# Optimization experiments

Hardware: AMD Instinct MI355X
Metric: run time of the kernel (lower is better)

Reference implementation:

```python
import jax, jax.numpy as jnp
import numpy as np

N = 8192
IN_C = 128
OUT_C = 64
ALPHA = 0.5  # LeakyReLU negative slope
NEG_INF = -9e15


def _xavier(key, shape, gain=1.414):
    fan_in, fan_out = shape[0], shape[-1]
    bound = gain * np.sqrt(6.0 / (fan_in + fan_out))
    return jax.random.uniform(key, shape, jnp.float32, -bound, bound)


def setup_inputs() -> dict:
    key = jax.random.key(0)
    k1, k2, k3, k4 = jax.random.split(key, 4)
    h = jax.random.normal(k1, (N, IN_C), jnp.float32)
    adj = jax.random.randint(k2, (N, N), 0, 2, jnp.int32)
    W = _xavier(k3, (IN_C, OUT_C))
    a = _xavier(k4, (2 * OUT_C, 1))
    return {"h": h, "adj": adj, "W": W, "a": a}


def reference(h, adj, W, a):
    # Wh: [N, out]
    Wh = h @ W
    a1 = a[:OUT_C, 0]   # [out]
    a2 = a[OUT_C:, 0]   # [out]
    # additive attention score e[i, j] = leakyrelu((Wh a1)_i + (Wh a2)_j)
    e = jax.nn.leaky_relu(
        (Wh @ a1)[:, None] + (Wh @ a2)[None, :], negative_slope=ALPHA
    )  # [N, N]
    scores = jnp.where(adj > 0, e, NEG_INF)
    attention = jax.nn.softmax(scores, axis=1)  # masked row softmax
    h_prime = attention @ Wh                    # [N, out]
    return jax.nn.leaky_relu(h_prime, negative_slope=ALPHA)  # concat=True path
```

## Files before the change

kernel.cpp:

```cpp
#include <hip/hip_runtime.h>
#include <hip/hip_bf16.h>

#define NN 8192
#define INC 128
#define OUTC 64

typedef __attribute__((ext_vector_type(8))) short bf16x8;
typedef __attribute__((ext_vector_type(4))) float f32x4;
typedef __attribute__((ext_vector_type(4))) int i32x4;

static __device__ __forceinline__ unsigned short f2bf(float x) {
    unsigned int u = __builtin_bit_cast(unsigned int, x);
    u += 0x7fffu + ((u >> 16) & 1u);
    return (unsigned short)(u >> 16);
}
static __device__ __forceinline__ float bf2f(unsigned short b) {
    unsigned int u = ((unsigned int)b) << 16;
    return __builtin_bit_cast(float, u);
}

__global__ __launch_bounds__(256) void k1_wh(const float* __restrict__ h,
                                             const float* __restrict__ W,
                                             const float* __restrict__ a,
                                             unsigned short* __restrict__ whbt,
                                             float* __restrict__ f,
                                             float* __restrict__ g)
{
    const int gid = blockIdx.x * 256 + threadIdx.x;
    const int row = gid >> 6;
    const int ch  = gid & 63;
    const f32x4* h4 = (const f32x4*)(h + (size_t)row * INC);
    float acc = 0.f;
#pragma unroll 8
    for (int k4 = 0; k4 < INC / 4; ++k4) {
        f32x4 hv = h4[k4];
        acc += hv[0] * W[(k4 * 4 + 0) * OUTC + ch];
        acc += hv[1] * W[(k4 * 4 + 1) * OUTC + ch];
        acc += hv[2] * W[(k4 * 4 + 2) * OUTC + ch];
        acc += hv[3] * W[(k4 * 4 + 3) * OUTC + ch];
    }
    whbt[(size_t)ch * NN + row] = f2bf(acc);

    float v1 = acc * a[ch];
    float v2 = acc * a[64 + ch];
#pragma unroll
    for (int m = 1; m < 64; m <<= 1) {
        v1 += __shfl_xor(v1, m, 64);
        v2 += __shfl_xor(v2, m, 64);
    }
    if ((threadIdx.x & 63) == 0) {
        f[row] = v1;
        g[row] = v2;
    }
}

__global__ __launch_bounds__(256) void k2_gmax(const float* __restrict__ g,
                                               float* __restrict__ gmax)
{
    __shared__ float red[256];
    float m = -1e30f;
    for (int i = threadIdx.x; i < NN; i += 256) m = fmaxf(m, g[i]);
    red[threadIdx.x] = m;
    __syncthreads();
    for (int s = 128; s > 0; s >>= 1) {
        if ((int)threadIdx.x < s) red[threadIdx.x] = fmaxf(red[threadIdx.x], red[threadIdx.x + s]);
        __syncthreads();
    }
    if (threadIdx.x == 0) *gmax = red[0];
}

__global__ __launch_bounds__(256) void k3_attn(const int* __restrict__ adj,
                                               const unsigned short* __restrict__ whbt,
                                               const float* __restrict__ f,
                                               const float* __restrict__ g,
                                               const float* __restrict__ gmaxp,
                                               float* __restrict__ accP,
                                               float* __restrict__ lP,
                                               int colsPerChunk)
{
    const int lane = threadIdx.x & 63;
    const int wave = threadIdx.x >> 6;
    const int lr16 = lane & 15;
    const int kg   = lane >> 4;
    const int rowBase = blockIdx.x * 64 + wave * 16;
    const int r = rowBase + lr16;
    const int chunk = blockIdx.y;
    const int jStart = chunk * colsPerChunk;

    const float L2E = 1.4426950408889634f;
    const float fr = f[r];
    const float gmax = *gmaxp;
    float mm = fr + gmax;
    mm = fmaxf(mm, 0.5f * mm);
    const float mL = mm * L2E;

    f32x4 acc0 = {0.f, 0.f, 0.f, 0.f};
    f32x4 acc1 = {0.f, 0.f, 0.f, 0.f};
    f32x4 acc2 = {0.f, 0.f, 0.f, 0.f};
    f32x4 acc3 = {0.f, 0.f, 0.f, 0.f};
    float ls = 0.f;

    const int* adjRow = adj + (size_t)r * NN;
    const unsigned short* wb0 = whbt + (size_t)(0 * 16 + lr16) * NN;
    const unsigned short* wb1 = whbt + (size_t)(1 * 16 + lr16) * NN;
    const unsigned short* wb2 = whbt + (size_t)(2 * 16 + lr16) * NN;
    const unsigned short* wb3 = whbt + (size_t)(3 * 16 + lr16) * NN;

    for (int j0 = jStart; j0 < jStart + colsPerChunk; j0 += 32) {
        const int jl = j0 + kg * 8;
        i32x4 ad0 = *(const i32x4*)(adjRow + jl);
        i32x4 ad1 = *(const i32x4*)(adjRow + jl + 4);
        f32x4 g0  = *(const f32x4*)(g + jl);
        f32x4 g1  = *(const f32x4*)(g + jl + 4);
        bf16x8 b0 = *(const bf16x8*)(wb0 + jl);
        bf16x8 b1 = *(const bf16x8*)(wb1 + jl);
        bf16x8 b2 = *(const bf16x8*)(wb2 + jl);
        bf16x8 b3 = *(const bf16x8*)(wb3 + jl);

        bf16x8 af;
#pragma unroll
        for (int t = 0; t < 8; ++t) {
            float gj = (t < 4) ? g0[t] : g1[t - 4];
            int   ad = (t < 4) ? ad0[t] : ad1[t - 4];
            float s  = fr + gj;
            float lr = fmaxf(s, 0.5f * s);
            float w  = __builtin_amdgcn_exp2f(lr * L2E - mL);
            w = (ad > 0) ? w : 0.f;
            unsigned short b = f2bf(w);
            af[t] = (short)b;
            ls += bf2f(b);
        }
        acc0 = __builtin_amdgcn_mfma_f32_16x16x32_bf16(af, b0, acc0, 0, 0, 0);
        acc1 = __builtin_amdgcn_mfma_f32_16x16x32_bf16(af, b1, acc1, 0, 0, 0);
        acc2 = __builtin_amdgcn_mfma_f32_16x16x32_bf16(af, b2, acc2, 0, 0, 0);
        acc3 = __builtin_amdgcn_mfma_f32_16x16x32_bf16(af, b3, acc3, 0, 0, 0);
    }

    ls += __shfl_xor(ls, 16, 64);
    ls += __shfl_xor(ls, 32, 64);
    if (lane < 16) lP[(size_t)chunk * NN + rowBase + lane] = ls;

    float* ap = accP + (size_t)chunk * NN * OUTC;
#pragma unroll
    for (int q = 0; q < 4; ++q) {
        const int rm = rowBase + kg * 4 + q;
        ap[(size_t)rm * OUTC +  0 + lr16] = acc0[q];
        ap[(size_t)rm * OUTC + 16 + lr16] = acc1[q];
        ap[(size_t)rm * OUTC + 32 + lr16] = acc2[q];
        ap[(size_t)rm * OUTC + 48 + lr16] = acc3[q];
    }
}

__global__ __launch_bounds__(256) void k4_final(const float* __restrict__ accP,
                                                const float* __restrict__ lP,
                                                float* __restrict__ out, int js)
{
    const int gid = blockIdx.x * 256 + threadIdx.x;
    const int row = gid >> 6;
    const int ch  = gid & 63;
    float av = 0.f, lv = 0.f;
    for (int c = 0; c < js; ++c) {
        av += accP[((size_t)c * NN + row) * OUTC + ch];
        lv += lP[(size_t)c * NN + row];
    }
    if (lv == 0.f) lv = 1.f;
    const float hv = av / lv;
    out[(size_t)row * OUTC + ch] = fmaxf(hv, 0.5f * hv);
}

extern "C" void kernel_launch(void* const* d_in, const int* in_sizes, int n_in,
                              void* d_out, int out_size, void* d_ws, size_t ws_size,
                              hipStream_t stream)
{
    const float* h   = (const float*)d_in[0];
    const int*   adj = (const int*)d_in[1];
    const float* W   = (const float*)d_in[2];
    const float* a   = (const float*)d_in[3];
    float* out = (float*)d_out;

    char* ws = (char*)d_ws;
    unsigned short* whbt = (unsigned short*)ws;
    size_t off = (size_t)OUTC * NN * sizeof(unsigned short);
    float* f = (float*)(ws + off); off += (size_t)NN * 4;
    float* g = (float*)(ws + off); off += (size_t)NN * 4;
    float* gmax = (float*)(ws + off); off += 256;

    const size_t perChunk = (size_t)NN * OUTC * 4 + (size_t)NN * 4;
    int js = 8;
    while (js > 1 && off + (size_t)js * perChunk > ws_size) js >>= 1;
    float* accP = (float*)(ws + off); off += (size_t)js * NN * OUTC * 4;
    float* lP   = (float*)(ws + off);

    k1_wh<<<dim3(NN * OUTC / 256), 256, 0, stream>>>(h, W, a, whbt, f, g);
    k2_gmax<<<1, 256, 0, stream>>>(g, gmax);
    const int colsPerChunk = NN / js;
    k3_attn<<<dim3(NN / 64, js), 256, 0, stream>>>(adj, whbt, f, g, gmax, accP, lP, colsPerChunk);
    k4_final<<<dim3(NN * OUTC / 256), 256, 0, stream>>>(accP, lP, out, js);
}
```

Baseline: 462.6 us.

## Pack adjacency into bitmask before attention kernel and coalesce Wh transpose stores

Adds a pre-pass that reads the int32 adjacency matrix once and packs it into a bitmask. The attention kernel then reads one 32-bit word per 32 columns instead of 32 ints, which cuts its adjacency traffic. k1 now transposes through shared memory so its Wh stores are vectorised, the column split doubles to 16 chunks, and the main loop is unrolled by 2. The full int32 adjacency is still read once, plus a 8 MB mask is written and read back, and k4 now has to reduce more partial chunks.

```diff
diff --git a/kernel.cpp b/kernel.cpp
--- a/kernel.cpp
+++ b/kernel.cpp
@@ -17,6 +17,28 @@
 static __device__ __forceinline__ float bf2f(unsigned short b) {
     unsigned int u = ((unsigned int)b) << 16;
     return __builtin_bit_cast(float, u);
+}
+
+__global__ __launch_bounds__(256) void ka_pack(const int* __restrict__ adj,
+                                               unsigned long long* __restrict__ msk)
+{
+    const int lane = threadIdx.x & 63;
+    const int wid  = (blockIdx.x * 256 + threadIdx.x) >> 6;
+    const int l16  = lane & 15;
+    const int g16  = lane >> 4;
+#pragma unroll 4
+    for (int i = 0; i < 32; ++i) {
+        const size_t base = ((size_t)wid * 32 + i) * 256;
+        i32x4 v = *(const i32x4*)(adj + base + 4 * lane);
+        unsigned int nib = (v[0] > 0 ? 1u : 0u) | (v[1] > 0 ? 2u : 0u)
+                         | (v[2] > 0 ? 4u : 0u) | (v[3] > 0 ? 8u : 0u);
+        unsigned long long m = (unsigned long long)nib << (4 * l16);
+        m |= __shfl_xor(m, 1, 64);
+        m |= __shfl_xor(m, 2, 64);
+        m |= __shfl_xor(m, 4, 64);
+        m |= __shfl_xor(m, 8, 64);
+        if (l16 == 0) msk[base / 64 + g16] = m;
+    }
 }
 
 __global__ __launch_bounds__(256) void k1_wh(const float* __restrict__ h,
@@ -26,9 +48,9 @@
                                              float* __restrict__ f,
                                              float* __restrict__ g)
 {
-    const int gid = blockIdx.x * 256 + threadIdx.x;
-    const int row = gid >> 6;
-    const int ch  = gid & 63;
+    const int wave = threadIdx.x >> 6;
+    const int ch   = threadIdx.x & 63;
+    const int row  = blockIdx.x * 4 + wave;
     const f32x4* h4 = (const f32x4*)(h + (size_t)row * INC);
     float acc = 0.f;
 #pragma unroll 8
@@ -39,7 +61,8 @@
         acc += hv[2] * W[(k4 * 4 + 2) * OUTC + ch];
         acc += hv[3] * W[(k4 * 4 + 3) * OUTC + ch];
     }
-    whbt[(size_t)ch * NN + row] = f2bf(acc);
+    __shared__ unsigned short tr[64][4];
+    tr[ch][wave] = f2bf(acc);
 
     float v1 = acc * a[ch];
     float v2 = acc * a[64 + ch];
@@ -48,9 +71,11 @@
         v1 += __shfl_xor(v1, m, 64);
         v2 += __shfl_xor(v2, m, 64);
     }
-    if ((threadIdx.x & 63) == 0) {
-        f[row] = v1;
-        g[row] = v2;
+    if (ch == 0) { f[row] = v1; g[row] = v2; }
+    __syncthreads();
+    if (wave == 0) {
+        ushort4 o = *(const ushort4*)&tr[ch][0];
+        *(ushort4*)(whbt + (size_t)ch * NN + blockIdx.x * 4) = o;
     }
 }
 
@@ -69,7 +94,7 @@
     if (threadIdx.x == 0) *gmax = red[0];
 }
 
-__global__ __launch_bounds__(256) void k3_attn(const int* __restrict__ adj,
+__global__ __launch_bounds__(256) void k3_attn(const unsigned int* __restrict__ msk,
                                                const unsigned short* __restrict__ whbt,
                                                const float* __restrict__ f,
                                                const float* __restrict__ g,
@@ -100,16 +125,17 @@
     f32x4 acc3 = {0.f, 0.f, 0.f, 0.f};
     float ls = 0.f;
 
-    const int* adjRow = adj + (size_t)r * NN;
+    const unsigned int* mrow = msk + (size_t)r * (NN / 32);
     const unsigned short* wb0 = whbt + (size_t)(0 * 16 + lr16) * NN;
     const unsigned short* wb1 = whbt + (size_t)(1 * 16 + lr16) * NN;
     const unsigned short* wb2 = whbt + (size_t)(2 * 16 + lr16) * NN;
     const unsigned short* wb3 = whbt + (size_t)(3 * 16 + lr16) * NN;
 
+#pragma unroll 2
     for (int j0 = jStart; j0 < jStart + colsPerChunk; j0 += 32) {
         const int jl = j0 + kg * 8;
-        i32x4 ad0 = *(const i32x4*)(adjRow + jl);
-        i32x4 ad1 = *(const i32x4*)(adjRow + jl + 4);
+        unsigned int mw = mrow[j0 >> 5];
+        unsigned int myb = (mw >> (kg * 8)) & 0xffu;
         f32x4 g0  = *(const f32x4*)(g + jl);
         f32x4 g1  = *(const f32x4*)(g + jl + 4);
         bf16x8 b0 = *(const bf16x8*)(wb0 + jl);
@@ -121,11 +147,10 @@
 #pragma unroll
         for (int t = 0; t < 8; ++t) {
             float gj = (t < 4) ? g0[t] : g1[t - 4];
-            int   ad = (t < 4) ? ad0[t] : ad1[t - 4];
             float s  = fr + gj;
             float lr = fmaxf(s, 0.5f * s);
             float w  = __builtin_amdgcn_exp2f(lr * L2E - mL);
-            w = (ad > 0) ? w : 0.f;
+            w = (myb & (1u << t)) ? w : 0.f;
             unsigned short b = f2bf(w);
             af[t] = (short)b;
             ls += bf2f(b);
@@ -184,16 +209,20 @@
     float* f = (float*)(ws + off); off += (size_t)NN * 4;
     float* g = (float*)(ws + off); off += (size_t)NN * 4;
     float* gmax = (float*)(ws + off); off += 256;
+    unsigned long long* msk = (unsigned long long*)(ws + off);
+    off += (size_t)NN * NN / 8;
 
     const size_t perChunk = (size_t)NN * OUTC * 4 + (size_t)NN * 4;
-    int js = 8;
+    int js = 16;
     while (js > 1 && off + (size_t)js * perChunk > ws_size) js >>= 1;
     float* accP = (float*)(ws + off); off += (size_t)js * NN * OUTC * 4;
     float* lP   = (float*)(ws + off);
 
-    k1_wh<<<dim3(NN * OUTC / 256), 256, 0, stream>>>(h, W, a, whbt, f, g);
+    ka_pack<<<dim3(2048), 256, 0, stream>>>(adj, msk);
+    k1_wh<<<dim3(NN / 4), 256, 0, stream>>>(h, W, a, whbt, f, g);
     k2_gmax<<<1, 256, 0, stream>>>(g, gmax);
     const int colsPerChunk = NN / js;
-    k3_attn<<<dim3(NN / 64, js), 256, 0, stream>>>(adj, whbt, f, g, gmax, accP, lP, colsPerChunk);
+    k3_attn<<<dim3(NN / 64, js), 256, 0, stream>>>((const unsigned int*)msk, whbt,
+                                                   f, g, gmax, accP, lP, colsPerChunk);
     k4_final<<<dim3(NN * OUTC / 256), 256, 0, stream>>>(accP, lP, out, js);
 }
```

New measurement: 483.5 us. +4.5%, slower.
